# Kernel optimization log

Hardware: AMD Instinct MI355X
Metric: run time of the kernel (lower is better)

Reference implementation:

```python
import jax, jax.numpy as jnp
import numpy as np

NUM_HEADS = 16


def setup_inputs() -> dict:
    key = jax.random.key(0)
    ks = jax.random.split(key, 8)
    S, B, E, L, P = 512, 32, 1024, 16, 10
    query = jax.random.normal(ks[0], (S, B, E), dtype=jnp.float32)
    prompt_ids = jax.random.randint(ks[1], (B, 1), 0, P, dtype=jnp.int32)
    batch_weight = jax.random.uniform(ks[2], (B,), dtype=jnp.float32)
    # xavier_uniform-like init for in_proj_weight
    bound = float(np.sqrt(6.0 / (3 * E + E)))
    in_proj_weight = jax.random.uniform(ks[3], (3 * E, E), minval=-bound, maxval=bound, dtype=jnp.float32)
    in_proj_bias = jnp.zeros((3 * E,), dtype=jnp.float32)
    ob = float(np.sqrt(6.0 / (E + E)))
    out_proj_weight = jax.random.uniform(ks[4], (E, E), minval=-ob, maxval=ob, dtype=jnp.float32)
    out_proj_bias = jnp.zeros((E,), dtype=jnp.float32)
    # prefix_pool: K-half uniform(-1,1), V-half zeros (as in torch init)
    pk = jax.random.uniform(ks[5], (P, 1, L, E), minval=-1.0, maxval=1.0, dtype=jnp.float32)
    prefix_pool = jnp.concatenate([pk, jnp.zeros((P, 1, L, E), dtype=jnp.float32)], axis=1)
    return {
        "query": query,
        "prompt_ids": prompt_ids,
        "batch_weight": batch_weight,
        "in_proj_weight": in_proj_weight,
        "in_proj_bias": in_proj_bias,
        "out_proj_weight": out_proj_weight,
        "out_proj_bias": out_proj_bias,
        "prefix_pool": prefix_pool,
    }


def _sdpa(q, k, v, scale):
    # q: [B,H,S,D], k/v: [B,H,T,D]
    scores = jnp.einsum("bhsd,bhtd->bhst", q, k) * scale
    probs = jax.nn.softmax(scores, axis=-1)
    return jnp.einsum("bhst,bhtd->bhsd", probs, v)


def reference(query, prompt_ids, batch_weight, in_proj_weight, in_proj_bias,
              out_proj_weight, out_proj_bias, prefix_pool):
    S, B, E = query.shape
    H = NUM_HEADS
    D = E // H
    scale = 1.0 / jnp.sqrt(jnp.asarray(D, dtype=query.dtype))

    # packed in-projection (q is k is v)
    qkv = query @ in_proj_weight.T + in_proj_bias          # [S,B,3E]
    q, k, v = jnp.split(qkv, 3, axis=-1)
    to_bhsd = lambda t: t.reshape(S, B, H, D).transpose(1, 2, 0, 3)  # [B,H,S,D]
    q, k, v = to_bhsd(q), to_bhsd(k), to_bhsd(v)

    # main attention
    attn = _sdpa(q, k, v, scale)                           # [B,H,S,D]

    # prefix attention
    prefix = prefix_pool[prompt_ids[:, 0]]                 # [B,2,L,E]
    L = prefix.shape[2]
    pk = prefix[:, 0].reshape(B, L, H, D).transpose(0, 2, 1, 3)  # [B,H,L,D]
    pv = prefix[:, 1].reshape(B, L, H, D).transpose(0, 2, 1, 3)
    attn_prefix = _sdpa(q, pk, pv, scale)                  # [B,H,S,D]
    attn_prefix = attn_prefix * batch_weight[:, None, None, None]

    out = attn + attn_prefix
    out = out.transpose(2, 0, 1, 3).reshape(S, B, E)       # [S,B,E]
    out = out @ out_proj_weight.T + out_proj_bias
    return out
```

## Files before the change

### kernel.cpp

```cpp
#include <hip/hip_runtime.h>
#include <stdint.h>

typedef unsigned short u16;
typedef __attribute__((ext_vector_type(8))) __bf16 bf16x8;
typedef __attribute__((ext_vector_type(4))) float f32x4;
typedef __attribute__((ext_vector_type(8))) unsigned short ushort8;

__device__ __forceinline__ u16 f2bf(float f) {
  unsigned int u = __builtin_bit_cast(unsigned int, f);
  return (u16)((u + 0x7fffu + ((u >> 16) & 1u)) >> 16);
}

__device__ __forceinline__ float fexp2(float x) {
  float r;
  asm volatile("v_exp_f32 %0, %1" : "=v"(r) : "v"(x));
  return r;
}

__device__ __forceinline__ f32x4 mfma16(bf16x8 a, bf16x8 b, f32x4 c) {
  return __builtin_amdgcn_mfma_f32_16x16x32_bf16(a, b, c, 0, 0, 0);
}

__device__ __forceinline__ void gload_lds16(const void* g, void* l) {
  __builtin_amdgcn_global_load_lds((const __attribute__((address_space(1))) void*)g,
                                   (__attribute__((address_space(3))) void*)l,
                                   16, 0, 0);
}

#define KSCALE 0.18033688011112294f

__global__ void __launch_bounds__(256) cvt_f32_bf16(const float* __restrict__ in,
                                                    u16* __restrict__ out, int n4) {
  int i = blockIdx.x * 256 + threadIdx.x;
  if (i >= n4) return;
  float4 v = ((const float4*)in)[i];
  u16* dst = out + (size_t)i * 4;
  dst[0] = f2bf(v.x); dst[1] = f2bf(v.y); dst[2] = f2bf(v.z); dst[3] = f2bf(v.w);
}

#define LDV(p) (*(const bf16x8*)(p))
#define RD_LO(AS, C) { aL[0]=LDV(AS+aRow+(C)); aL[1]=LDV(AS+aRow+1024+(C)); \
                       aL[2]=LDV(AS+aRow+2048+(C)); aL[3]=LDV(AS+aRow+3072+(C)); }
#define RD_HI(AS, C) { aH[0]=LDV(AS+aRow+4096+(C)); aH[1]=LDV(AS+aRow+5120+(C)); \
                       aH[2]=LDV(AS+aRow+6144+(C)); aH[3]=LDV(AS+aRow+7168+(C)); }
#define RD_B(BS, R, C) { R[0]=LDV(BS+bRow+(C)); R[1]=LDV(BS+bRow+1024+(C)); \
                         R[2]=LDV(BS+bRow+2048+(C)); R[3]=LDV(BS+bRow+3072+(C)); }
#define STA(DST, Q, T) gload_lds16(baseA + (Q)*K64 + (size_t)(T)*64, (DST) + (Q)*4096 + stDst)
#define STB(DST, Q, T) gload_lds16(baseB + (Q)*K64 + (size_t)(T)*64, (DST) + (Q)*4096 + stDst)
#define MM_LO(BB) { _Pragma("unroll") for (int mi=0;mi<4;++mi) \
                    _Pragma("unroll") for (int ni=0;ni<4;++ni) \
                      acc[mi][ni]=mfma16(aL[mi],(BB)[ni],acc[mi][ni]); }
#define MM_HI(BB) { _Pragma("unroll") for (int mi=0;mi<4;++mi) \
                    _Pragma("unroll") for (int ni=0;ni<4;++ni) \
                      acc[mi+4][ni]=mfma16(aH[mi],(BB)[ni],acc[mi+4][ni]); }
#define VMW(N) asm volatile("s_waitcnt vmcnt(" #N ")" ::: "memory")
#define BAR() __builtin_amdgcn_s_barrier()
#define LK0() { asm volatile("s_waitcnt lgkmcnt(0)" ::: "memory"); \
                __builtin_amdgcn_sched_barrier(0); }
#define PRIO1() __builtin_amdgcn_s_setprio(1)
#define PRIO0() __builtin_amdgcn_s_setprio(0)
#define MFMA_PH(MM, BB) { PRIO1(); MM(BB); PRIO0(); }

template <int MODE>
__global__ void __launch_bounds__(512, 2) gemm8p(
    const u16* __restrict__ A, const u16* __restrict__ B,
    const float* __restrict__ bias, void* __restrict__ Cout,
    u16* __restrict__ q_out, u16* __restrict__ k_out, u16* __restrict__ v_out,
    int M, int N, int K) {
  __shared__ alignas(16) u16 As[2][16384];
  __shared__ alignas(16) u16 Bs[2][16384];

  const int tid = threadIdx.x;
  const int w = tid >> 6, l = tid & 63;
  const int wm = w >> 2, wn = w & 3;
  const long bm = (long)blockIdx.x * 256;
  const long bn = (long)blockIdx.y * 256;
  const int NT = K >> 6;
  const int NIT = NT >> 1;

  const int srow = w * 8 + (l >> 3);
  const int schk = ((l & 7) ^ (l >> 3)) * 8;
  const u16* baseA = A + (bm + srow) * (size_t)K + schk;
  const u16* baseB = B + (bn + srow) * (size_t)K + schk;
  const size_t K64 = (size_t)K * 64;
  const int stDst = w * 512;

  u16* const as0 = &As[0][0]; u16* const as1 = &As[1][0];
  u16* const bs0 = &Bs[0][0]; u16* const bs1 = &Bs[1][0];

  const int fr = l & 15, fkg = l >> 4;
  const int sw = (fr & 7) << 3;
  const int c0 = (fkg * 8) ^ sw;
  const int c1 = (32 + fkg * 8) ^ sw;
  const int aRow = (wm * 128 + fr) * 64;
  const int bRow = (wn * 64 + fr) * 64;

  f32x4 acc[8][4] = {};
  bf16x8 aL[4], aH[4], b0[4], b1[4];

  STB(bs0, 0, 0); STB(bs0, 1, 0);
  STB(bs0, 2, 0); STB(bs0, 3, 0);
  STA(as0, 0, 0); STA(as0, 2, 0);
  STA(as0, 1, 0); STA(as0, 3, 0);
  STB(bs1, 0, 1); STB(bs1, 1, 1);
  VMW(4); BAR();

  for (int it = 0; it < NIT - 1; ++it) {
    const int t1 = 2 * it + 1, t2 = 2 * it + 2, t3 = 2 * it + 3;
    RD_LO(as0, c0); RD_B(bs0, b0, c0);
    STB(bs1, 2, t1); STB(bs1, 3, t1);
    VMW(4); BAR(); LK0(); MFMA_PH(MM_LO, b0); BAR();
    RD_HI(as0, c0);
    STA(as1, 0, t1); STA(as1, 2, t1);
    BAR(); LK0(); MFMA_PH(MM_HI, b0); BAR();
    RD_LO(as0, c1); RD_B(bs0, b1, c1);
    STA(as1, 1, t1); STA(as1, 3, t1);
    BAR(); LK0(); MFMA_PH(MM_LO, b1); BAR();
    RD_HI(as0, c1);
    STB(bs0, 0, t2); STB(bs0, 1, t2);
    VMW(4); BAR(); LK0(); MFMA_PH(MM_HI, b1); BAR();
    RD_LO(as1, c0); RD_B(bs1, b0, c0);
    STB(bs0, 2, t2); STB(bs0, 3, t2);
    VMW(4); BAR(); LK0(); MFMA_PH(MM_LO, b0); BAR();
    RD_HI(as1, c0);
    STA(as0, 0, t2); STA(as0, 2, t2);
    BAR(); LK0(); MFMA_PH(MM_HI, b0); BAR();
    RD_LO(as1, c1); RD_B(bs1, b1, c1);
    STA(as0, 1, t2); STA(as0, 3, t2);
    BAR(); LK0(); MFMA_PH(MM_LO, b1); BAR();
    RD_HI(as1, c1);
    STB(bs1, 0, t3); STB(bs1, 1, t3);
    VMW(4); BAR(); LK0(); MFMA_PH(MM_HI, b1); BAR();
  }
  {
    const int t1 = NT - 1;
    RD_LO(as0, c0); RD_B(bs0, b0, c0);
    STB(bs1, 2, t1); STB(bs1, 3, t1);
    VMW(4); BAR(); LK0(); MFMA_PH(MM_LO, b0); BAR();
    RD_HI(as0, c0);
    STA(as1, 0, t1); STA(as1, 2, t1);
    BAR(); LK0(); MFMA_PH(MM_HI, b0); BAR();
    RD_LO(as0, c1); RD_B(bs0, b1, c1);
    STA(as1, 1, t1); STA(as1, 3, t1);
    BAR(); LK0(); MFMA_PH(MM_LO, b1); BAR();
    RD_HI(as0, c1);
    VMW(2); BAR(); LK0(); MFMA_PH(MM_HI, b1); BAR();
    RD_LO(as1, c0); RD_B(bs1, b0, c0);
    VMW(0); BAR(); LK0(); MFMA_PH(MM_LO, b0); BAR();
    RD_HI(as1, c0);
    BAR(); LK0(); MFMA_PH(MM_HI, b0); BAR();
    RD_LO(as1, c1); RD_B(bs1, b1, c1);
    BAR(); LK0(); MFMA_PH(MM_LO, b1); BAR();
    RD_HI(as1, c1);
    BAR(); LK0(); MFMA_PH(MM_HI, b1);
  }

  const int r0 = wm * 128 + ((l >> 4) << 2);
  const int cc0 = wn * 64 + (l & 15);
#pragma unroll
  for (int mi = 0; mi < 8; ++mi) {
#pragma unroll
    for (int j = 0; j < 4; ++j) {
      long r = bm + r0 + mi * 16 + j;
#pragma unroll
      for (int ni = 0; ni < 4; ++ni) {
        long c = bn + cc0 + ni * 16;
        float v = acc[mi][ni][j] + bias[c];
        if (MODE == 0) {
          ((float*)Cout)[r * N + c] = v;
        } else {
          int s = (int)(r >> 5), bb = (int)(r & 31);
          int sec = (int)(c >> 10), e = (int)(c & 1023);
          int hh = e >> 6, d = e & 63;
          if (sec == 0) v *= KSCALE;
          u16* dst = (sec == 0) ? q_out : (sec == 1) ? k_out : v_out;
          dst[(((size_t)(bb * 16 + hh) * 512 + s) * 64) + d] = f2bf(v);
        }
      }
    }
  }
}

__global__ void __launch_bounds__(1024, 4) attn_v4(
    const u16* __restrict__ Q, const u16* __restrict__ K, const u16* __restrict__ V,
    const float* __restrict__ prefix_pool, const int* __restrict__ prompt_ids,
    const float* __restrict__ batch_weight, u16* __restrict__ attn_out) {
  constexpr int E = 1024, L = 16;
  const int h = blockIdx.x, b = blockIdx.y;
  const int tid = threadIdx.x;
  const int wid = tid >> 6, lane = tid & 63;
  const int fr = lane & 15, fkg = lane >> 4;

  __shared__ alignas(16) u16 Ks[64 * 64];
  __shared__ alignas(16) u16 VTs[64 * 64];
  __shared__ alignas(16) u16 Ps[16][16 * 64];
  __shared__ alignas(16) u16 pKs[L * 64];
  __shared__ alignas(16) u16 pVTs[64 * 32];

  const size_t bh = (size_t)(b * 16 + h);
  const u16* Kbase = K + bh * 512 * 64;
  const u16* Vbase = V + bh * 512 * 64;
  const u16* Qbase = Q + bh * 512 * 64;
  const int q0 = wid * 32;

  const bool isK = (tid < 512);
  const int st = isK ? tid : tid - 512;
  const int srow = st >> 3;
  const int scol = (st & 7) * 8;
  const u16* sbase = (isK ? Kbase : Vbase) + srow * 64 + scol;

  ushort8 stgA, stgB;
  stgA = *(const ushort8*)(sbase);

  const int pid = prompt_ids[b];
  const float* pk = prefix_pool + ((size_t)pid * 2 * L) * E + h * 64;
  const float* pv = pk + (size_t)L * E;
  if (tid < 256) {
    int ll = tid >> 4, d0 = (tid & 15) * 4;
    float4 v = *(const float4*)(pk + (size_t)ll * E + d0);
    u16 t4[4] = {f2bf(v.x), f2bf(v.y), f2bf(v.z), f2bf(v.w)};
#pragma unroll
    for (int i = 0; i < 4; ++i)
      pKs[(ll * 64 + d0 + i) ^ ((ll & 7) << 3)] = t4[i];
  } else if (tid < 512) {
    int t = tid - 256;
    int d = t >> 2, kv0 = (t & 3) * 8;
#pragma unroll
    for (int i = 0; i < 8; ++i) {
      int kv = kv0 + i;
      float v = (kv < L) ? pv[(size_t)kv * E + d] : 0.f;
      pVTs[d * 32 + kv] = f2bf(v);
    }
  }

  bf16x8 qf[2][2];
#pragma unroll
  for (int mt = 0; mt < 2; ++mt) {
    int qrow = q0 + mt * 16 + fr;
    qf[mt][0] = *(const bf16x8*)(Qbase + qrow * 64 + fkg * 8);
    qf[mt][1] = *(const bf16x8*)(Qbase + qrow * 64 + 32 + fkg * 8);
  }

  float m2[2] = {-3e38f, -3e38f}, lsum[2] = {0.f, 0.f};
  f32x4 oacc[2][4] = {};
  u16* const pw = Ps[wid];
  const int psw = (fr & 7) << 3;

#define STAGE_WRITE(STG)                                                      \
  if (isK) {                                                                  \
    int e = (srow * 64 + scol) ^ ((srow & 7) << 3);                           \
    *(ushort8*)(Ks + e) = STG;                                                \
  } else {                                                                    \
    _Pragma("unroll") for (int i = 0; i < 8; ++i) {                           \
      int d = scol + i;                                                       \
      VTs[(d * 64 + srow) ^ ((d & 7) << 3)] = STG[i];                         \
    }                                                                         \
  }

#define COMPUTE(CC)                                                           \
  _Pragma("unroll") for (int mt = 0; mt < 2; ++mt) {                          \
    f32x4 sa[4];                                                              \
    _Pragma("unroll") for (int nt = 0; nt < 4; ++nt) {                        \
      int krow = nt * 16 + fr;                                                \
      int kb = krow * 64, swz = (krow & 7) << 3;                              \
      bf16x8 kf0 = *(const bf16x8*)(Ks + ((kb + fkg * 8) ^ swz));             \
      bf16x8 kf1 = *(const bf16x8*)(Ks + ((kb + 32 + fkg * 8) ^ swz));        \
      f32x4 z = {};                                                           \
      sa[nt] = mfma16(kf0, qf[mt][0], z);                                     \
      sa[nt] = mfma16(kf1, qf[mt][1], sa[nt]);                                \
    }                                                                         \
    float mx = sa[0][0];                                                      \
    _Pragma("unroll") for (int nt = 0; nt < 4; ++nt)                          \
      _Pragma("unroll") for (int j = 0; j < 4; ++j)                           \
        mx = fmaxf(mx, sa[nt][j]);                                            \
    mx = fmaxf(mx, __shfl_xor(mx, 16, 64));                                   \
    mx = fmaxf(mx, __shfl_xor(mx, 32, 64));                                   \
    if (!__all(mx <= m2[mt] + 8.0f)) {                                        \
      float mnew = fmaxf(m2[mt], mx);                                         \
      float al = fexp2(m2[mt] - mnew);                                        \
      lsum[mt] *= al;                                                         \
      _Pragma("unroll") for (int j = 0; j < 4; ++j) {                         \
        float alj = __shfl(al, fkg * 4 + j, 64);                              \
        _Pragma("unroll") for (int t = 0; t < 4; ++t) oacc[mt][t][j] *= alj;  \
      }                                                                       \
      m2[mt] = mnew;                                                          \
    }                                                                         \
    float sum = 0.f;                                                          \
    _Pragma("unroll") for (int nt = 0; nt < 4; ++nt)                          \
      _Pragma("unroll") for (int j = 0; j < 4; ++j) {                         \
        float p = fexp2(sa[nt][j] - m2[mt]);                                  \
        sa[nt][j] = p;                                                        \
        sum += p;                                                             \
      }                                                                       \
    sum += __shfl_xor(sum, 16, 64);                                           \
    sum += __shfl_xor(sum, 32, 64);                                           \
    lsum[mt] += sum;                                                          \
    _Pragma("unroll") for (int nt = 0; nt < 4; ++nt)                          \
      _Pragma("unroll") for (int i = 0; i < 2; ++i) {                         \
        unsigned int pack = (unsigned int)f2bf(sa[nt][2 * i]) |               \
                            ((unsigned int)f2bf(sa[nt][2 * i + 1]) << 16);    \
        int kv = nt * 16 + fkg * 4 + 2 * i;                                   \
        *(unsigned int*)(pw + fr * 64 + (kv ^ psw)) = pack;                   \
      }                                                                       \
    _Pragma("unroll") for (int kk = 0; kk < 2; ++kk) {                        \
      bf16x8 pa = *(const bf16x8*)(pw + fr * 64 + ((kk * 32 + fkg * 8) ^ psw)); \
      _Pragma("unroll") for (int t = 0; t < 4; ++t) {                         \
        int vd = t * 16 + fr;                                                 \
        bf16x8 vf = *(const bf16x8*)(VTs + ((vd * 64 + kk * 32 + fkg * 8) ^ ((vd & 7) << 3))); \
        oacc[mt][t] = mfma16(pa, vf, oacc[mt][t]);                            \
      }                                                                       \
    }                                                                         \
  }

#define CHUNK(CUR, NXT, C)                                                    \
  {                                                                           \
    STAGE_WRITE(CUR);                                                         \
    if ((C) < 7) NXT = *(const ushort8*)(sbase + ((C) + 1) * 4096);           \
    __syncthreads();                                                          \
    COMPUTE(C);                                                               \
    __syncthreads();                                                          \
  }

  CHUNK(stgA, stgB, 0);
  CHUNK(stgB, stgA, 1);
  CHUNK(stgA, stgB, 2);
  CHUNK(stgB, stgA, 3);
  CHUNK(stgA, stgB, 4);
  CHUNK(stgB, stgA, 5);
  CHUNK(stgA, stgB, 6);
  CHUNK(stgB, stgA, 7);

  const float bw = batch_weight[b];
#pragma unroll
  for (int mt = 0; mt < 2; ++mt) {
    f32x4 sp;
    {
      int swz = (fr & 7) << 3;
      bf16x8 a0 = *(const bf16x8*)(pKs + ((fr * 64 + fkg * 8) ^ swz));
      bf16x8 a1 = *(const bf16x8*)(pKs + ((fr * 64 + 32 + fkg * 8) ^ swz));
      f32x4 z = {};
      sp = mfma16(a0, qf[mt][0], z);
      sp = mfma16(a1, qf[mt][1], sp);
    }
    float mx = fmaxf(fmaxf(sp[0], sp[1]), fmaxf(sp[2], sp[3]));
    mx = fmaxf(mx, __shfl_xor(mx, 16, 64));
    mx = fmaxf(mx, __shfl_xor(mx, 32, 64));
    float psum = 0.f;
#pragma unroll
    for (int j = 0; j < 4; ++j) {
      float p = fexp2(sp[j] - mx);
      sp[j] = p;
      psum += p;
    }
    psum += __shfl_xor(psum, 16, 64);
    psum += __shfl_xor(psum, 32, 64);
#pragma unroll
    for (int i = 0; i < 2; ++i) {
      unsigned int pack = (unsigned int)f2bf(sp[2 * i]) |
                          ((unsigned int)f2bf(sp[2 * i + 1]) << 16);
      int kv = fkg * 4 + 2 * i;
      *(unsigned int*)(pw + fr * 64 + (kv ^ psw)) = pack;
      int kv2 = 16 + fkg * 4 + 2 * i;
      *(unsigned int*)(pw + fr * 64 + (kv2 ^ psw)) = 0u;
    }
    f32x4 op[4] = {};
    {
      bf16x8 pa = *(const bf16x8*)(pw + fr * 64 + ((fkg * 8) ^ psw));
#pragma unroll
      for (int t = 0; t < 4; ++t) {
        bf16x8 vf = *(const bf16x8*)(pVTs + (t * 16 + fr) * 32 + fkg * 8);
        op[t] = mfma16(pa, vf, op[t]);
      }
    }
#pragma unroll
    for (int j = 0; j < 4; ++j) {
      float lj = __shfl(lsum[mt], fkg * 4 + j, 64);
      float lpj = __shfl(psum, fkg * 4 + j, 64);
      int s = q0 + mt * 16 + fkg * 4 + j;
      size_t m = (size_t)s * 32 + b;
      float invl = 1.f / lj, invlp = 1.f / lpj;
#pragma unroll
      for (int t = 0; t < 4; ++t) {
        float v = oacc[mt][t][j] * invl + bw * op[t][j] * invlp;
        attn_out[m * E + h * 64 + t * 16 + fr] = f2bf(v);
      }
    }
  }
}

extern "C" void kernel_launch(void* const* d_in, const int* in_sizes, int n_in,
                              void* d_out, int out_size, void* d_ws, size_t ws_size,
                              hipStream_t stream) {
  const float* query = (const float*)d_in[0];
  const int* prompt_ids = (const int*)d_in[1];
  const float* batch_weight = (const float*)d_in[2];
  const float* in_proj_w = (const float*)d_in[3];
  const float* in_proj_b = (const float*)d_in[4];
  const float* out_proj_w = (const float*)d_in[5];
  const float* out_proj_b = (const float*)d_in[6];
  const float* prefix_pool = (const float*)d_in[7];
  float* out = (float*)d_out;

  u16* qbf = (u16*)d_ws;
  u16* wqkv = qbf + (size_t)16384 * 1024;
  u16* wout = wqkv + (size_t)3072 * 1024;
  u16* qx = wout + (size_t)1024 * 1024;
  u16* kx = qx + (size_t)32 * 16 * 512 * 64;
  u16* vx = kx + (size_t)32 * 16 * 512 * 64;
  u16* attnb = vx + (size_t)32 * 16 * 512 * 64;

  cvt_f32_bf16<<<16384, 256, 0, stream>>>(query, qbf, 16384 * 1024 / 4);
  cvt_f32_bf16<<<3072, 256, 0, stream>>>(in_proj_w, wqkv, 3072 * 1024 / 4);
  cvt_f32_bf16<<<1024, 256, 0, stream>>>(out_proj_w, wout, 1024 * 1024 / 4);

  gemm8p<2><<<dim3(64, 12), 512, 0, stream>>>(qbf, wqkv, in_proj_b, nullptr,
                                              qx, kx, vx, 16384, 3072, 1024);
  attn_v4<<<dim3(16, 32), 1024, 0, stream>>>(qx, kx, vx, prefix_pool, prompt_ids,
                                             batch_weight, attnb);
  gemm8p<0><<<dim3(64, 4), 512, 0, stream>>>(attnb, wout, out_proj_b, out,
                                             nullptr, nullptr, nullptr,
                                             16384, 1024, 1024);
}
```

Measured before the change: 268.0 us.

## Swizzle GEMM block order across XCDs and issue tile prefetches earlier

```diff
diff --git a/kernel.cpp b/kernel.cpp
--- a/kernel.cpp
+++ b/kernel.cpp
@@ -60,6 +60,7 @@
 #define PRIO1() __builtin_amdgcn_s_setprio(1)
 #define PRIO0() __builtin_amdgcn_s_setprio(0)
 #define MFMA_PH(MM, BB) { PRIO1(); MM(BB); PRIO0(); }
+#define TAIL(MM, BB) { BAR(); LK0(); MFMA_PH(MM, BB); BAR(); }
 
 template <int MODE>
 __global__ void __launch_bounds__(512, 2) gemm8p(
@@ -73,8 +74,15 @@
   const int tid = threadIdx.x;
   const int w = tid >> 6, l = tid & 63;
   const int wm = w >> 2, wn = w & 3;
-  const long bm = (long)blockIdx.x * 256;
-  const long bn = (long)blockIdx.y * 256;
+
+  const int nwg = gridDim.x;
+  const int lin = blockIdx.x;
+  const int cpx = nwg >> 3;
+  const int swz = (lin & 7) * cpx + (lin >> 3);
+  const int mTiles = M >> 8;
+  const long bm = (long)(swz % mTiles) * 256;
+  const long bn = (long)(swz / mTiles) * 256;
+
   const int NT = K >> 6;
   const int NIT = NT >> 1;
 
@@ -98,59 +106,61 @@
   f32x4 acc[8][4] = {};
   bf16x8 aL[4], aH[4], b0[4], b1[4];
 
-  STB(bs0, 0, 0); STB(bs0, 1, 0);
-  STB(bs0, 2, 0); STB(bs0, 3, 0);
-  STA(as0, 0, 0); STA(as0, 2, 0);
-  STA(as0, 1, 0); STA(as0, 3, 0);
+  STA(as0, 0, 0); STA(as0, 1, 0); STA(as0, 2, 0); STA(as0, 3, 0);
+  STB(bs0, 0, 0); STB(bs0, 1, 0); STB(bs0, 2, 0); STB(bs0, 3, 0);
+  STA(as1, 0, 1); STA(as1, 2, 1);
   STB(bs1, 0, 1); STB(bs1, 1, 1);
   VMW(4); BAR();
 
   for (int it = 0; it < NIT - 1; ++it) {
     const int t1 = 2 * it + 1, t2 = 2 * it + 2, t3 = 2 * it + 3;
+    STA(as1, 1, t1); STA(as1, 3, t1);
+    STB(bs1, 2, t1); STB(bs1, 3, t1);
     RD_LO(as0, c0); RD_B(bs0, b0, c0);
-    STB(bs1, 2, t1); STB(bs1, 3, t1);
-    VMW(4); BAR(); LK0(); MFMA_PH(MM_LO, b0); BAR();
+    TAIL(MM_LO, b0);
     RD_HI(as0, c0);
-    STA(as1, 0, t1); STA(as1, 2, t1);
-    BAR(); LK0(); MFMA_PH(MM_HI, b0); BAR();
+    TAIL(MM_HI, b0);
     RD_LO(as0, c1); RD_B(bs0, b1, c1);
-    STA(as1, 1, t1); STA(as1, 3, t1);
-    BAR(); LK0(); MFMA_PH(MM_LO, b1); BAR();
+    TAIL(MM_LO, b1);
+    STA(as0, 0, t2); STA(as0, 2, t2);
+    STB(bs0, 0, t2); STB(bs0, 1, t2);
+    VMW(4);
     RD_HI(as0, c1);
-    STB(bs0, 0, t2); STB(bs0, 1, t2);
-    VMW(4); BAR(); LK0(); MFMA_PH(MM_HI, b1); BAR();
+    TAIL(MM_HI, b1);
+    STA(as0, 1, t2); STA(as0, 3, t2);
+    STB(bs0, 2, t2); STB(bs0, 3, t2);
     RD_LO(as1, c0); RD_B(bs1, b0, c0);
-    STB(bs0, 2, t2); STB(bs0, 3, t2);
-    VMW(4); BAR(); LK0(); MFMA_PH(MM_LO, b0); BAR();
+    TAIL(MM_LO, b0);
     RD_HI(as1, c0);
-    STA(as0, 0, t2); STA(as0, 2, t2);
-    BAR(); LK0(); MFMA_PH(MM_HI, b0); BAR();
+    TAIL(MM_HI, b0);
     RD_LO(as1, c1); RD_B(bs1, b1, c1);
-    STA(as0, 1, t2); STA(as0, 3, t2);
-    BAR(); LK0(); MFMA_PH(MM_LO, b1); BAR();
+    TAIL(MM_LO, b1);
+    STA(as1, 0, t3); STA(as1, 2, t3);
+    STB(bs1, 0, t3); STB(bs1, 1, t3);
+    VMW(4);
     RD_HI(as1, c1);
-    STB(bs1, 0, t3); STB(bs1, 1, t3);
-    VMW(4); BAR(); LK0(); MFMA_PH(MM_HI, b1); BAR();
-  }
+    TAIL(MM_HI, b1);
+  }
+
   {
     const int t1 = NT - 1;
+    STA(as1, 1, t1); STA(as1, 3, t1);
+    STB(bs1, 2, t1); STB(bs1, 3, t1);
     RD_LO(as0, c0); RD_B(bs0, b0, c0);
-    STB(bs1, 2, t1); STB(bs1, 3, t1);
-    VMW(4); BAR(); LK0(); MFMA_PH(MM_LO, b0); BAR();
+    TAIL(MM_LO, b0);
     RD_HI(as0, c0);
-    STA(as1, 0, t1); STA(as1, 2, t1);
-    BAR(); LK0(); MFMA_PH(MM_HI, b0); BAR();
+    TAIL(MM_HI, b0);
     RD_LO(as0, c1); RD_B(bs0, b1, c1);
-    STA(as1, 1, t1); STA(as1, 3, t1);
-    BAR(); LK0(); MFMA_PH(MM_LO, b1); BAR();
+    TAIL(MM_LO, b1);
+    VMW(0);
     RD_HI(as0, c1);
-    VMW(2); BAR(); LK0(); MFMA_PH(MM_HI, b1); BAR();
+    TAIL(MM_HI, b1);
     RD_LO(as1, c0); RD_B(bs1, b0, c0);
-    VMW(0); BAR(); LK0(); MFMA_PH(MM_LO, b0); BAR();
+    TAIL(MM_LO, b0);
     RD_HI(as1, c0);
-    BAR(); LK0(); MFMA_PH(MM_HI, b0); BAR();
+    TAIL(MM_HI, b0);
     RD_LO(as1, c1); RD_B(bs1, b1, c1);
-    BAR(); LK0(); MFMA_PH(MM_LO, b1); BAR();
+    TAIL(MM_LO, b1);
     RD_HI(as1, c1);
     BAR(); LK0(); MFMA_PH(MM_HI, b1);
   }
@@ -413,11 +423,11 @@
   cvt_f32_bf16<<<3072, 256, 0, stream>>>(in_proj_w, wqkv, 3072 * 1024 / 4);
   cvt_f32_bf16<<<1024, 256, 0, stream>>>(out_proj_w, wout, 1024 * 1024 / 4);
 
-  gemm8p<2><<<dim3(64, 12), 512, 0, stream>>>(qbf, wqkv, in_proj_b, nullptr,
-                                              qx, kx, vx, 16384, 3072, 1024);
+  gemm8p<2><<<768, 512, 0, stream>>>(qbf, wqkv, in_proj_b, nullptr,
+                                     qx, kx, vx, 16384, 3072, 1024);
   attn_v4<<<dim3(16, 32), 1024, 0, stream>>>(qx, kx, vx, prefix_pool, prompt_ids,
                                              batch_weight, attnb);
-  gemm8p<0><<<dim3(64, 4), 512, 0, stream>>>(attnb, wout, out_proj_b, out,
-                                             nullptr, nullptr, nullptr,
-                                             16384, 1024, 1024);
-}
+  gemm8p<0><<<256, 512, 0, stream>>>(attnb, wout, out_proj_b, out,
+                                     nullptr, nullptr, nullptr,
+                                     16384, 1024, 1024);
+}
```

Result: no change. 270.5 us (+0.9%).
